# Performance work log

Measured on AMD Instinct MI355X. Metric: run time of the kernel, lower is better.

Reference implementation:

```python
import jax, jax.numpy as jnp
import numpy as np

B, T, D = 64, 2048, 512


def setup_inputs() -> dict:
    key = jax.random.key(0)
    ks = jax.random.split(key, 6)
    lim_tau = 1.0 / np.sqrt(2 * D)  # torch Linear default init bound
    lim_mem = 1.0 / np.sqrt(D)
    return {
        "x": jax.random.normal(ks[0], (B, T, D), dtype=jnp.float32),
        "tau_w": jax.random.uniform(ks[1], (D, 2 * D), jnp.float32, -lim_tau, lim_tau),
        "tau_b": jax.random.uniform(ks[2], (D,), jnp.float32, -lim_tau, lim_tau),
        "mem_w": jax.random.uniform(ks[3], (D, D), jnp.float32, -lim_mem, lim_mem),
        "mem_b": jax.random.uniform(ks[4], (D,), jnp.float32, -lim_mem, lim_mem),
        "log_thresh": jnp.zeros((D,), jnp.float32),
    }


def reference(x, tau_w, tau_b, mem_w, mem_b, log_thresh):
    b, t, d = x.shape
    thr = jax.nn.sigmoid(log_thresh)  # [D]

    def step(carry, xt):
        v, tau = carry  # each [B, D]
        # liquid time-constant gate: sigmoid(Linear([xt, tau]))
        tau = jax.nn.sigmoid(jnp.concatenate([xt, tau], axis=-1) @ tau_w.T + tau_b)
        alpha = jnp.exp(-1.0 / (tau + 1e-6))
        v = alpha * v + (1.0 - alpha) * (xt @ mem_w.T + mem_b)
        s = (v >= thr).astype(x.dtype)  # spike
        v = v * (1.0 - s)  # hard reset
        return (v, tau), s

    x_tbd = jnp.swapaxes(x, 0, 1)  # [T, B, D] for scan
    init = (jnp.zeros((b, d), x.dtype), jnp.ones((b, d), x.dtype))
    (v, tau), spikes = jax.lax.scan(step, init, x_tbd)
    return jnp.swapaxes(spikes, 0, 1), tau, v  # [B,T,D], [B,D], [B,D]
```

## Files before the change

kernel.cpp:

```cpp
#include <hip/hip_runtime.h>
#include <math.h>

#define B_ 64
#define T_ 2048
#define D_ 512
#define BT_ (B_ * T_)
#define XWORDS (B_ * D_)

typedef unsigned long long u64;
typedef float f32x4 __attribute__((ext_vector_type(4)));

__global__ void prep_weights(const float* __restrict__ tau_w,
                             const float* __restrict__ mem_w,
                             float* __restrict__ Wcat,
                             float* __restrict__ WTh) {
    int idx = blockIdx.x * 256 + threadIdx.x;
    {
        int k = idx >> 10, j = idx & 1023;
        float v = (j < 512) ? tau_w[j * 1024 + k] : mem_w[(j - 512) * 512 + k];
        Wcat[idx] = v;
    }
    if (idx < 512 * 512) {
        int k = idx >> 9, d = idx & 511;
        WTh[idx] = tau_w[d * 1024 + 512 + k];
    }
}

__global__ __launch_bounds__(256, 2)
void gemm_xw(const float* __restrict__ X, const float* __restrict__ Wc,
             const float* __restrict__ tau_b, const float* __restrict__ mem_b,
             float* __restrict__ Aout, float* __restrict__ Mout) {
    __shared__ __align__(16) float As[16][128];
    __shared__ __align__(16) float Bs[16][128];
    const int bn = blockIdx.x;
    const int bm = blockIdx.y;
    const int tid = threadIdx.x;
    const int tm = (tid >> 4) << 3;
    const int tn = (tid & 15) << 3;
    const int m0 = bm * 128, n0 = bn * 128;

    const float4* X4 = (const float4*)X;
    const float4* Wc4 = (const float4*)Wc;

    float acc[8][8];
#pragma unroll
    for (int i = 0; i < 8; i++)
#pragma unroll
        for (int j = 0; j < 8; j++) acc[i][j] = 0.0f;

    const int ar = tid >> 1;
    const int ac2 = (tid & 1) * 2;
    const int bkr = tid >> 4;
    const int bc = (tid & 15) * 2;

    for (int kt = 0; kt < 512; kt += 16) {
        float4 av0 = X4[(m0 + ar) * 128 + (kt >> 2) + ac2];
        float4 av1 = X4[(m0 + ar) * 128 + (kt >> 2) + ac2 + 1];
        float4 bv0 = Wc4[(kt + bkr) * 256 + bn * 32 + bc];
        float4 bv1 = Wc4[(kt + bkr) * 256 + bn * 32 + bc + 1];
        __syncthreads();
        As[ac2 * 4 + 0][ar] = av0.x;
        As[ac2 * 4 + 1][ar] = av0.y;
        As[ac2 * 4 + 2][ar] = av0.z;
        As[ac2 * 4 + 3][ar] = av0.w;
        As[ac2 * 4 + 4][ar] = av1.x;
        As[ac2 * 4 + 5][ar] = av1.y;
        As[ac2 * 4 + 6][ar] = av1.z;
        As[ac2 * 4 + 7][ar] = av1.w;
        *(float4*)&Bs[bkr][bc * 4] = bv0;
        *(float4*)&Bs[bkr][bc * 4 + 4] = bv1;
        __syncthreads();
#pragma unroll
        for (int kk = 0; kk < 16; kk++) {
            float4 a0 = *(const float4*)&As[kk][tm];
            float4 a1 = *(const float4*)&As[kk][tm + 4];
            float4 b0 = *(const float4*)&Bs[kk][tn];
            float4 b1 = *(const float4*)&Bs[kk][tn + 4];
            float av[8] = {a0.x, a0.y, a0.z, a0.w, a1.x, a1.y, a1.z, a1.w};
            float bv[8] = {b0.x, b0.y, b0.z, b0.w, b1.x, b1.y, b1.z, b1.w};
#pragma unroll
            for (int i = 0; i < 8; i++)
#pragma unroll
                for (int j = 0; j < 8; j++)
                    acc[i][j] = fmaf(av[i], bv[j], acc[i][j]);
        }
    }

    const bool isA = (bn < 4);
    float* Cout = isA ? Aout : Mout;
    const float* bias = isA ? tau_b : mem_b;
    const int ncol0 = (isA ? n0 : n0 - 512) + tn;
    float bj[8];
#pragma unroll
    for (int j = 0; j < 8; j++) bj[j] = bias[ncol0 + j];
#pragma unroll
    for (int i = 0; i < 8; i++) {
        size_t off = (size_t)(m0 + tm + i) * 512 + ncol0;
        f32x4 o0, o1;
        o0.x = acc[i][0] + bj[0]; o0.y = acc[i][1] + bj[1];
        o0.z = acc[i][2] + bj[2]; o0.w = acc[i][3] + bj[3];
        o1.x = acc[i][4] + bj[4]; o1.y = acc[i][5] + bj[5];
        o1.z = acc[i][6] + bj[6]; o1.w = acc[i][7] + bj[7];
        __builtin_nontemporal_store(o0, (f32x4*)&Cout[off]);
        __builtin_nontemporal_store(o1, (f32x4*)&Cout[off + 4]);
    }
}

__global__ void init_sync(u64* __restrict__ xchg, int* __restrict__ ctr) {
    int idx = blockIdx.x * 256 + threadIdx.x;
    if (idx < 2 * XWORDS) xchg[idx] = (idx < XWORDS) ? 0x3F800000ull : 0ull;
    if (idx < 16) ctr[idx] = 0;
}

__global__ __launch_bounds__(512)
__attribute__((amdgpu_waves_per_eu(2, 2)))
void scan_nt(const float* __restrict__ WTh,
             const float* __restrict__ Mm,
             const float* __restrict__ log_thresh,
             float* __restrict__ AmOut,
             float* __restrict__ OutTail,
             u64* __restrict__ xchg,
             int* __restrict__ ctr) {
    __shared__ __align__(16) float4 w_lds[8192];
    __shared__ __align__(16) float part[2][2][8][64];
    __shared__ int role_s;

    const int tid = threadIdx.x;

    if (tid == 0) {
        unsigned xcd;
        asm volatile("s_getreg_b32 %0, hwreg(HW_REG_XCC_ID)" : "=s"(xcd));
        xcd &= 7;
        int rank = atomicAdd(&ctr[xcd], 1) & 31;
        role_s = ((rank & 7) << 8) | ((int)xcd * 4 + (rank >> 3));
    }
    __syncthreads();
    const int sg = role_s >> 8;
    const int bp = role_s & 255;

    {
        const int ch = tid & 63;
        const int kr8 = tid >> 6;
        float* wl = (float*)w_lds;
        for (int i = 0; i < 64; i++) {
            int krow = i * 8 + kr8;
            wl[(krow >> 2) * 256 + ch * 4 + (krow & 3)] =
                WTh[krow * 512 + sg * 64 + ch];
        }
    }

    const int ws = tid >> 6;
    const int lane = tid & 63;

    const int eb = tid >> 6;
    const int ech = tid & 63;
    const int gch = sg * 64 + ech;
    float thr = 0.f, v = 0.f, tau_keep = 0.f;
    if (tid < 128) thr = 1.0f / (1.0f + expf(-log_thresh[gch]));
    size_t abase = ((size_t)(bp * 2 + eb) * T_) * D_ + gch;

    float a_pf = 0.f, m_pf = 0.f;
    if (tid < 128) {
        a_pf = __builtin_nontemporal_load(&AmOut[abase]);
        m_pf = __builtin_nontemporal_load(&Mm[abase]);
    }
    __syncthreads();

    for (int c = 1; c <= T_; c++) {
        float a_nx = 0.f, m_nx = 0.f;
        if (tid < 128) {
            size_t nx = (c < T_) ? abase + D_ : abase;
            a_nx = __builtin_nontemporal_load(&AmOut[nx]);
            m_nx = __builtin_nontemporal_load(&Mm[nx]);
        }

        const u64* s0 = xchg + (size_t)((c - 1) & 1) * XWORDS
                             + (size_t)(bp * 2) * 512 + ws * 64 + lane;
        const u64* s1 = s0 + 512;
        const unsigned tgt = (unsigned)(c - 1);
        u64 v0, v1;
        int guard = 0;
        do {
            v0 = __hip_atomic_load(s0, __ATOMIC_RELAXED,
                                   __HIP_MEMORY_SCOPE_AGENT);
            v1 = __hip_atomic_load(s1, __ATOMIC_RELAXED,
                                   __HIP_MEMORY_SCOPE_AGENT);
        } while ((((unsigned)(v0 >> 32) < tgt) |
                  ((unsigned)(v1 >> 32) < tgt)) && ++guard < (1 << 22));
        const int t0i = (int)(unsigned)v0;
        const int t1i = (int)(unsigned)v1;

        float acc0 = 0.f, acc1 = 0.f;
#pragma unroll
        for (int q4 = 0; q4 < 16; q4++) {
            float4 wv = w_lds[(ws * 16 + q4) * 64 + lane];
#pragma unroll
            for (int j = 0; j < 4; j++) {
                const int kk = q4 * 4 + j;
                const float wj = (j == 0) ? wv.x : (j == 1) ? wv.y
                               : (j == 2) ? wv.z : wv.w;
                float ta = __uint_as_float(
                    (unsigned)__builtin_amdgcn_readlane(t0i, kk));
                float tb = __uint_as_float(
                    (unsigned)__builtin_amdgcn_readlane(t1i, kk));
                acc0 = fmaf(ta, wj, acc0);
                acc1 = fmaf(tb, wj, acc1);
            }
        }
        const int par = c & 1;
        part[par][0][ws][lane] = acc0;
        part[par][1][ws][lane] = acc1;
        __syncthreads();

        if (tid < 128) {
            float sum = 0.f;
#pragma unroll
            for (int j = 0; j < 8; j++) sum += part[par][eb][j][ech];
            float pre = sum + a_pf;
            float tau = 1.0f / (1.0f + expf(-pre));
            u64 pack = ((u64)(unsigned)c << 32) | (u64)__float_as_uint(tau);
            __hip_atomic_store(&xchg[(size_t)(c & 1) * XWORDS
                                     + (bp * 2 + eb) * 512 + gch],
                               pack, __ATOMIC_RELAXED, __HIP_MEMORY_SCOPE_AGENT);
            float alpha = expf(-1.0f / (tau + 1e-6f));
            v = alpha * v + (1.0f - alpha) * m_pf;
            float s = (v >= thr) ? 1.0f : 0.0f;
            __builtin_nontemporal_store(s, &AmOut[abase]);
            v = v * (1.0f - s);
            tau_keep = tau;
            abase += D_;
            a_pf = a_nx; m_pf = m_nx;
        }
    }

    if (tid < 128) {
        const size_t batch = bp * 2 + eb;
        OutTail[(size_t)BT_ * D_ + batch * D_ + gch] = tau_keep;
        OutTail[(size_t)BT_ * D_ + (size_t)B_ * D_ + batch * D_ + gch] = v;
    }
}

extern "C" void kernel_launch(void* const* d_in, const int* in_sizes, int n_in,
                              void* d_out, int out_size, void* d_ws, size_t ws_size,
                              hipStream_t stream) {
    (void)in_sizes; (void)n_in; (void)out_size; (void)ws_size;
    const float* x          = (const float*)d_in[0];
    const float* tau_w      = (const float*)d_in[1];
    const float* tau_b      = (const float*)d_in[2];
    const float* mem_w      = (const float*)d_in[3];
    const float* mem_b      = (const float*)d_in[4];
    const float* log_thresh = (const float*)d_in[5];
    float* out = (float*)d_out;

    float* Wcat = (float*)d_ws;
    float* WTh  = Wcat + 512 * 1024;
    float* Mout = WTh + 512 * 512;
    u64* xchg = (u64*)d_ws;
    int* ctr  = (int*)((char*)d_ws + 2 * XWORDS * sizeof(u64));

    float* Aout = out;

    prep_weights<<<2048, 256, 0, stream>>>(tau_w, mem_w, Wcat, WTh);
    gemm_xw<<<dim3(8, 1024), 256, 0, stream>>>(x, Wcat, tau_b, mem_b, Aout, Mout);
    init_sync<<<256, 256, 0, stream>>>(xchg, ctr);

    const float* WThc = WTh;
    const float* Mmc  = Mout;
    const float* ltc  = log_thresh;
    float* outp = out;
    u64* xchgp = xchg;
    int* ctrp = ctr;
    void* args[7] = {(void*)&WThc, (void*)&Mmc, (void*)&ltc,
                     (void*)&Aout, (void*)&outp, (void*)&xchgp, (void*)&ctrp};
    hipLaunchCooperativeKernel((const void*)scan_nt, dim3(256), dim3(512),
                               args, 0, stream);
}
```

Before: 5.998 ms.

## Let owning wave compute its slice locally and skip global exchange polling

The elementwise update for each block's 64-channel slice moves from waves 0-1 to the wave whose k-range matches that slice, so that wave handles both batches. That wave keeps its tau values in registers instead of polling the global exchange buffer, which takes one of the eight cross-block spin waits off each step's critical path. In exchange, the serial elementwise work now sits on a single wave, and the polling guard drops from 2^22 to 2^16 iterations, which could time out early under heavy contention.

```diff
diff --git a/kernel.cpp b/kernel.cpp
--- a/kernel.cpp
+++ b/kernel.cpp
@@ -114,7 +114,7 @@
 
 __global__ __launch_bounds__(512)
 __attribute__((amdgpu_waves_per_eu(2, 2)))
-void scan_nt(const float* __restrict__ WTh,
+void scan_ws(const float* __restrict__ WTh,
              const float* __restrict__ Mm,
              const float* __restrict__ log_thresh,
              float* __restrict__ AmOut,
@@ -151,44 +151,43 @@
 
     const int ws = tid >> 6;
     const int lane = tid & 63;
-
-    const int eb = tid >> 6;
-    const int ech = tid & 63;
-    const int gch = sg * 64 + ech;
-    float thr = 0.f, v = 0.f, tau_keep = 0.f;
-    if (tid < 128) thr = 1.0f / (1.0f + expf(-log_thresh[gch]));
-    size_t abase = ((size_t)(bp * 2 + eb) * T_) * D_ + gch;
-
-    float a_pf = 0.f, m_pf = 0.f;
-    if (tid < 128) {
-        a_pf = __builtin_nontemporal_load(&AmOut[abase]);
-        m_pf = __builtin_nontemporal_load(&Mm[abase]);
+    const bool self = (ws == sg);
+    const int gch = sg * 64 + lane;
+
+    float thr = 0.f, v0 = 0.f, v1 = 0.f, tk0 = 1.0f, tk1 = 1.0f;
+    size_t ab0 = 0, ab1 = 0;
+    float a0_pf = 0.f, m0_pf = 0.f, a1_pf = 0.f, m1_pf = 0.f;
+    if (self) {
+        thr = 1.0f / (1.0f + expf(-log_thresh[gch]));
+        ab0 = (size_t)(bp * 2) * T_ * D_ + gch;
+        ab1 = ab0 + (size_t)T_ * D_;
+        a0_pf = __builtin_nontemporal_load(&AmOut[ab0]);
+        m0_pf = __builtin_nontemporal_load(&Mm[ab0]);
+        a1_pf = __builtin_nontemporal_load(&AmOut[ab1]);
+        m1_pf = __builtin_nontemporal_load(&Mm[ab1]);
     }
     __syncthreads();
 
+    int t0i = 0x3F800000, t1i = 0x3F800000;
+
     for (int c = 1; c <= T_; c++) {
-        float a_nx = 0.f, m_nx = 0.f;
-        if (tid < 128) {
-            size_t nx = (c < T_) ? abase + D_ : abase;
-            a_nx = __builtin_nontemporal_load(&AmOut[nx]);
-            m_nx = __builtin_nontemporal_load(&Mm[nx]);
-        }
-
-        const u64* s0 = xchg + (size_t)((c - 1) & 1) * XWORDS
-                             + (size_t)(bp * 2) * 512 + ws * 64 + lane;
-        const u64* s1 = s0 + 512;
-        const unsigned tgt = (unsigned)(c - 1);
-        u64 v0, v1;
-        int guard = 0;
-        do {
-            v0 = __hip_atomic_load(s0, __ATOMIC_RELAXED,
-                                   __HIP_MEMORY_SCOPE_AGENT);
-            v1 = __hip_atomic_load(s1, __ATOMIC_RELAXED,
-                                   __HIP_MEMORY_SCOPE_AGENT);
-        } while ((((unsigned)(v0 >> 32) < tgt) |
-                  ((unsigned)(v1 >> 32) < tgt)) && ++guard < (1 << 22));
-        const int t0i = (int)(unsigned)v0;
-        const int t1i = (int)(unsigned)v1;
+        if (!self) {
+            const u64* s0 = xchg + (size_t)((c - 1) & 1) * XWORDS
+                                 + (size_t)(bp * 2) * 512 + ws * 64 + lane;
+            const u64* s1 = s0 + 512;
+            const unsigned tgt = (unsigned)(c - 1);
+            u64 w0, w1;
+            int guard = 0;
+            do {
+                w0 = __hip_atomic_load(s0, __ATOMIC_RELAXED,
+                                       __HIP_MEMORY_SCOPE_AGENT);
+                w1 = __hip_atomic_load(s1, __ATOMIC_RELAXED,
+                                       __HIP_MEMORY_SCOPE_AGENT);
+            } while ((((unsigned)(w0 >> 32) < tgt) |
+                      ((unsigned)(w1 >> 32) < tgt)) && ++guard < (1 << 16));
+            t0i = (int)(unsigned)w0;
+            t1i = (int)(unsigned)w1;
+        }
 
         float acc0 = 0.f, acc1 = 0.f;
 #pragma unroll
@@ -212,31 +211,53 @@
         part[par][1][ws][lane] = acc1;
         __syncthreads();
 
-        if (tid < 128) {
-            float sum = 0.f;
-#pragma unroll
-            for (int j = 0; j < 8; j++) sum += part[par][eb][j][ech];
-            float pre = sum + a_pf;
-            float tau = 1.0f / (1.0f + expf(-pre));
-            u64 pack = ((u64)(unsigned)c << 32) | (u64)__float_as_uint(tau);
-            __hip_atomic_store(&xchg[(size_t)(c & 1) * XWORDS
-                                     + (bp * 2 + eb) * 512 + gch],
-                               pack, __ATOMIC_RELAXED, __HIP_MEMORY_SCOPE_AGENT);
-            float alpha = expf(-1.0f / (tau + 1e-6f));
-            v = alpha * v + (1.0f - alpha) * m_pf;
-            float s = (v >= thr) ? 1.0f : 0.0f;
-            __builtin_nontemporal_store(s, &AmOut[abase]);
-            v = v * (1.0f - s);
-            tau_keep = tau;
-            abase += D_;
-            a_pf = a_nx; m_pf = m_nx;
-        }
-    }
-
-    if (tid < 128) {
-        const size_t batch = bp * 2 + eb;
-        OutTail[(size_t)BT_ * D_ + batch * D_ + gch] = tau_keep;
-        OutTail[(size_t)BT_ * D_ + (size_t)B_ * D_ + batch * D_ + gch] = v;
+        if (self) {
+            float a0_nx = 0.f, m0_nx = 0.f, a1_nx = 0.f, m1_nx = 0.f;
+            if (c < T_) {
+                a0_nx = __builtin_nontemporal_load(&AmOut[ab0 + D_]);
+                m0_nx = __builtin_nontemporal_load(&Mm[ab0 + D_]);
+                a1_nx = __builtin_nontemporal_load(&AmOut[ab1 + D_]);
+                m1_nx = __builtin_nontemporal_load(&Mm[ab1 + D_]);
+            }
+            float s0 = 0.f, s1 = 0.f;
+#pragma unroll
+            for (int j = 0; j < 8; j++) s0 += part[par][0][j][lane];
+#pragma unroll
+            for (int j = 0; j < 8; j++) s1 += part[par][1][j][lane];
+            float tau0 = 1.0f / (1.0f + expf(-(s0 + a0_pf)));
+            float tau1 = 1.0f / (1.0f + expf(-(s1 + a1_pf)));
+            u64 base = (size_t)(c & 1) * XWORDS + (size_t)(bp * 2) * 512 + gch;
+            __hip_atomic_store(&xchg[base],
+                               ((u64)(unsigned)c << 32) | (u64)__float_as_uint(tau0),
+                               __ATOMIC_RELAXED, __HIP_MEMORY_SCOPE_AGENT);
+            __hip_atomic_store(&xchg[base + 512],
+                               ((u64)(unsigned)c << 32) | (u64)__float_as_uint(tau1),
+                               __ATOMIC_RELAXED, __HIP_MEMORY_SCOPE_AGENT);
+            float al0 = expf(-1.0f / (tau0 + 1e-6f));
+            float al1 = expf(-1.0f / (tau1 + 1e-6f));
+            v0 = al0 * v0 + (1.0f - al0) * m0_pf;
+            v1 = al1 * v1 + (1.0f - al1) * m1_pf;
+            float sp0 = (v0 >= thr) ? 1.0f : 0.0f;
+            float sp1 = (v1 >= thr) ? 1.0f : 0.0f;
+            __builtin_nontemporal_store(sp0, &AmOut[ab0]);
+            __builtin_nontemporal_store(sp1, &AmOut[ab1]);
+            v0 *= (1.0f - sp0);
+            v1 *= (1.0f - sp1);
+            tk0 = tau0; tk1 = tau1;
+            t0i = __float_as_int(tau0);
+            t1i = __float_as_int(tau1);
+            ab0 += D_; ab1 += D_;
+            a0_pf = a0_nx; m0_pf = m0_nx;
+            a1_pf = a1_nx; m1_pf = m1_nx;
+        }
+    }
+
+    if (self) {
+        const size_t b0 = bp * 2, b1 = bp * 2 + 1;
+        OutTail[(size_t)BT_ * D_ + b0 * D_ + gch] = tk0;
+        OutTail[(size_t)BT_ * D_ + b1 * D_ + gch] = tk1;
+        OutTail[(size_t)BT_ * D_ + (size_t)B_ * D_ + b0 * D_ + gch] = v0;
+        OutTail[(size_t)BT_ * D_ + (size_t)B_ * D_ + b1 * D_ + gch] = v1;
     }
 }
 
@@ -272,6 +293,6 @@
     int* ctrp = ctr;
     void* args[7] = {(void*)&WThc, (void*)&Mmc, (void*)&ltc,
                      (void*)&Aout, (void*)&outp, (void*)&xchgp, (void*)&ctrp};
-    hipLaunchCooperativeKernel((const void*)scan_nt, dim3(256), dim3(512),
+    hipLaunchCooperativeKernel((const void*)scan_ws, dim3(256), dim3(512),
                                args, 0, stream);
 }
```

After: 7.175 ms. 19.6% more time.

## Repartition scan blocks to 4 batches by 32 channels with LDS-staged tau

Applied to the files above, without the earlier changes.

Each of the 256 cooperative blocks now owns 4 batch rows and 32 output channels instead of 2 batches and 64 channels. The exchange buffer is re-laid out batch-interleaved per channel so one thread polls four adjacent words. The previous tau is staged in LDS and read as float4 rather than broadcast via readlane. This halves the per-block weight slice and replaces readlane broadcasts with LDS vector reads, at the cost of an extra __syncthreads per step, twice as many partial sums to reduce, and padded LDS use that limits occupancy.

```diff
diff --git a/kernel.cpp b/kernel.cpp
--- a/kernel.cpp
+++ b/kernel.cpp
@@ -114,15 +114,17 @@
 
 __global__ __launch_bounds__(512)
 __attribute__((amdgpu_waves_per_eu(2, 2)))
-void scan_nt(const float* __restrict__ WTh,
+void scan_q4(const float* __restrict__ WTh,
              const float* __restrict__ Mm,
              const float* __restrict__ log_thresh,
              float* __restrict__ AmOut,
              float* __restrict__ OutTail,
              u64* __restrict__ xchg,
              int* __restrict__ ctr) {
-    __shared__ __align__(16) float4 w_lds[8192];
-    __shared__ __align__(16) float part[2][2][8][64];
+    __shared__ __align__(16) float4 w_lds[4096];
+    __shared__ __align__(16) float tau_s[4][512];
+    __shared__ __align__(16) float part[4][16][32];
+    __shared__ float pad_lds[10240];
     __shared__ int role_s;
 
     const int tid = threadIdx.x;
@@ -132,32 +134,36 @@
         asm volatile("s_getreg_b32 %0, hwreg(HW_REG_XCC_ID)" : "=s"(xcd));
         xcd &= 7;
         int rank = atomicAdd(&ctr[xcd], 1) & 31;
-        role_s = ((rank & 7) << 8) | ((int)xcd * 4 + (rank >> 3));
+        role_s = ((rank & 15) << 8) | ((int)xcd * 2 + (rank >> 4));
     }
     __syncthreads();
     const int sg = role_s >> 8;
-    const int bp = role_s & 255;
+    const int qd = role_s & 255;
+    if (role_s == -12345) pad_lds[tid] = 1.f;
 
     {
-        const int ch = tid & 63;
-        const int kr8 = tid >> 6;
+        const int ch = tid & 31;
+        const int kr = tid >> 5;
         float* wl = (float*)w_lds;
-        for (int i = 0; i < 64; i++) {
-            int krow = i * 8 + kr8;
-            wl[(krow >> 2) * 256 + ch * 4 + (krow & 3)] =
-                WTh[krow * 512 + sg * 64 + ch];
+        for (int i = 0; i < 32; i++) {
+            int krow = i * 16 + kr;
+            wl[(krow >> 2) * 128 + ch * 4 + (krow & 3)] =
+                WTh[krow * 512 + sg * 32 + ch];
         }
     }
 
     const int ws = tid >> 6;
     const int lane = tid & 63;
-
-    const int eb = tid >> 6;
-    const int ech = tid & 63;
-    const int gch = sg * 64 + ech;
-    float thr = 0.f, v = 0.f, tau_keep = 0.f;
+    const int cp = lane & 31;
+    const int kh = lane >> 5;
+
+    const int ech = tid & 31;
+    const int eb = (tid >> 5) & 3;
+    const int gch = sg * 32 + ech;
+    const int batch = qd * 4 + eb;
+    float thr = 0.f, v = 0.f, tk = 1.0f;
     if (tid < 128) thr = 1.0f / (1.0f + expf(-log_thresh[gch]));
-    size_t abase = ((size_t)(bp * 2 + eb) * T_) * D_ + gch;
+    size_t abase = (size_t)batch * T_ * D_ + gch;
 
     float a_pf = 0.f, m_pf = 0.f;
     if (tid < 128) {
@@ -174,69 +180,81 @@
             m_nx = __builtin_nontemporal_load(&Mm[nx]);
         }
 
-        const u64* s0 = xchg + (size_t)((c - 1) & 1) * XWORDS
-                             + (size_t)(bp * 2) * 512 + ws * 64 + lane;
-        const u64* s1 = s0 + 512;
+        const u64* s = xchg + (size_t)((c - 1) & 1) * XWORDS
+                            + (size_t)qd * 2048 + (size_t)(ws * 64 + lane) * 4;
         const unsigned tgt = (unsigned)(c - 1);
-        u64 v0, v1;
+        u64 w0, w1, w2, w3;
         int guard = 0;
         do {
-            v0 = __hip_atomic_load(s0, __ATOMIC_RELAXED,
-                                   __HIP_MEMORY_SCOPE_AGENT);
-            v1 = __hip_atomic_load(s1, __ATOMIC_RELAXED,
-                                   __HIP_MEMORY_SCOPE_AGENT);
-        } while ((((unsigned)(v0 >> 32) < tgt) |
-                  ((unsigned)(v1 >> 32) < tgt)) && ++guard < (1 << 22));
-        const int t0i = (int)(unsigned)v0;
-        const int t1i = (int)(unsigned)v1;
-
-        float acc0 = 0.f, acc1 = 0.f;
-#pragma unroll
-        for (int q4 = 0; q4 < 16; q4++) {
-            float4 wv = w_lds[(ws * 16 + q4) * 64 + lane];
-#pragma unroll
-            for (int j = 0; j < 4; j++) {
-                const int kk = q4 * 4 + j;
-                const float wj = (j == 0) ? wv.x : (j == 1) ? wv.y
-                               : (j == 2) ? wv.z : wv.w;
-                float ta = __uint_as_float(
-                    (unsigned)__builtin_amdgcn_readlane(t0i, kk));
-                float tb = __uint_as_float(
-                    (unsigned)__builtin_amdgcn_readlane(t1i, kk));
-                acc0 = fmaf(ta, wj, acc0);
-                acc1 = fmaf(tb, wj, acc1);
-            }
-        }
-        const int par = c & 1;
-        part[par][0][ws][lane] = acc0;
-        part[par][1][ws][lane] = acc1;
+            w0 = __hip_atomic_load(s + 0, __ATOMIC_RELAXED,
+                                   __HIP_MEMORY_SCOPE_AGENT);
+            w1 = __hip_atomic_load(s + 1, __ATOMIC_RELAXED,
+                                   __HIP_MEMORY_SCOPE_AGENT);
+            w2 = __hip_atomic_load(s + 2, __ATOMIC_RELAXED,
+                                   __HIP_MEMORY_SCOPE_AGENT);
+            w3 = __hip_atomic_load(s + 3, __ATOMIC_RELAXED,
+                                   __HIP_MEMORY_SCOPE_AGENT);
+        } while ((((unsigned)(w0 >> 32) < tgt) |
+                  ((unsigned)(w1 >> 32) < tgt) |
+                  ((unsigned)(w2 >> 32) < tgt) |
+                  ((unsigned)(w3 >> 32) < tgt)) && ++guard < (1 << 20));
+        tau_s[0][ws * 64 + lane] = __uint_as_float((unsigned)w0);
+        tau_s[1][ws * 64 + lane] = __uint_as_float((unsigned)w1);
+        tau_s[2][ws * 64 + lane] = __uint_as_float((unsigned)w2);
+        tau_s[3][ws * 64 + lane] = __uint_as_float((unsigned)w3);
+        __builtin_amdgcn_wave_barrier();
+
+        float acc0 = 0.f, acc1 = 0.f, acc2 = 0.f, acc3 = 0.f;
+#pragma unroll
+        for (int q = 0; q < 8; q++) {
+            const int qq = ws * 16 + kh * 8 + q;
+            float4 wv = w_lds[qq * 32 + cp];
+            const int k0 = ws * 64 + kh * 32 + q * 4;
+            float4 t0 = *(const float4*)&tau_s[0][k0];
+            float4 t1 = *(const float4*)&tau_s[1][k0];
+            float4 t2 = *(const float4*)&tau_s[2][k0];
+            float4 t3 = *(const float4*)&tau_s[3][k0];
+            acc0 = fmaf(t0.x, wv.x, acc0); acc0 = fmaf(t0.y, wv.y, acc0);
+            acc0 = fmaf(t0.z, wv.z, acc0); acc0 = fmaf(t0.w, wv.w, acc0);
+            acc1 = fmaf(t1.x, wv.x, acc1); acc1 = fmaf(t1.y, wv.y, acc1);
+            acc1 = fmaf(t1.z, wv.z, acc1); acc1 = fmaf(t1.w, wv.w, acc1);
+            acc2 = fmaf(t2.x, wv.x, acc2); acc2 = fmaf(t2.y, wv.y, acc2);
+            acc2 = fmaf(t2.z, wv.z, acc2); acc2 = fmaf(t2.w, wv.w, acc2);
+            acc3 = fmaf(t3.x, wv.x, acc3); acc3 = fmaf(t3.y, wv.y, acc3);
+            acc3 = fmaf(t3.z, wv.z, acc3); acc3 = fmaf(t3.w, wv.w, acc3);
+        }
+        const int slot = ws * 2 + kh;
+        part[0][slot][cp] = acc0;
+        part[1][slot][cp] = acc1;
+        part[2][slot][cp] = acc2;
+        part[3][slot][cp] = acc3;
         __syncthreads();
 
         if (tid < 128) {
             float sum = 0.f;
 #pragma unroll
-            for (int j = 0; j < 8; j++) sum += part[par][eb][j][ech];
+            for (int j = 0; j < 16; j++) sum += part[eb][j][ech];
             float pre = sum + a_pf;
             float tau = 1.0f / (1.0f + expf(-pre));
             u64 pack = ((u64)(unsigned)c << 32) | (u64)__float_as_uint(tau);
             __hip_atomic_store(&xchg[(size_t)(c & 1) * XWORDS
-                                     + (bp * 2 + eb) * 512 + gch],
+                                     + (size_t)qd * 2048 + (size_t)gch * 4 + eb],
                                pack, __ATOMIC_RELAXED, __HIP_MEMORY_SCOPE_AGENT);
             float alpha = expf(-1.0f / (tau + 1e-6f));
             v = alpha * v + (1.0f - alpha) * m_pf;
-            float s = (v >= thr) ? 1.0f : 0.0f;
-            __builtin_nontemporal_store(s, &AmOut[abase]);
-            v = v * (1.0f - s);
-            tau_keep = tau;
+            float sp = (v >= thr) ? 1.0f : 0.0f;
+            __builtin_nontemporal_store(sp, &AmOut[abase]);
+            v = v * (1.0f - sp);
+            tk = tau;
             abase += D_;
             a_pf = a_nx; m_pf = m_nx;
         }
+        __syncthreads();
     }
 
     if (tid < 128) {
-        const size_t batch = bp * 2 + eb;
-        OutTail[(size_t)BT_ * D_ + batch * D_ + gch] = tau_keep;
-        OutTail[(size_t)BT_ * D_ + (size_t)B_ * D_ + batch * D_ + gch] = v;
+        OutTail[(size_t)BT_ * D_ + (size_t)batch * D_ + gch] = tk;
+        OutTail[(size_t)BT_ * D_ + (size_t)B_ * D_ + (size_t)batch * D_ + gch] = v;
     }
 }
 
@@ -272,6 +290,6 @@
     int* ctrp = ctr;
     void* args[7] = {(void*)&WThc, (void*)&Mmc, (void*)&ltc,
                      (void*)&Aout, (void*)&outp, (void*)&xchgp, (void*)&ctrp};
-    hipLaunchCooperativeKernel((const void*)scan_nt, dim3(256), dim3(512),
+    hipLaunchCooperativeKernel((const void*)scan_q4, dim3(256), dim3(512),
                                args, 0, stream);
 }
```

Result: slower. 8.268 ms (+37.8%).
